# Performance work log

Measured on AMD Instinct MI355X. Metric: run time of the kernel, lower is better.

Reference implementation:

```python
import jax, jax.numpy as jnp
import numpy as np
from jax import lax

WIN = 7
PAD = WIN // 2
K1, K2 = 0.01, 0.03
NP = WIN * WIN
COV_NORM = NP / (NP - 1)  # use_sample_covariance=True


def _dwconv(x, w, channel):
    # depthwise 2D conv, SAME-style explicit padding (torch conv2d padding=pad)
    return lax.conv_general_dilated(
        x, w, window_strides=(1, 1),
        padding=[(PAD, PAD), (PAD, PAD)],
        feature_group_count=channel,
        dimension_numbers=('NCHW', 'OIHW', 'NCHW'))


def setup_inputs() -> dict:
    key = jax.random.key(0)
    k1, k2 = jax.random.split(key)
    B, C, H, W = 64, 1, 384, 384
    gt = jax.random.uniform(k1, (B, C, H, W), dtype=jnp.float32)
    pred = jax.random.uniform(k2, (B, C, H, W), dtype=jnp.float32)
    # uniform (box) window: create_window(7, channel=1, gaussian_weights=False)
    window = jnp.ones((C, 1, WIN, WIN), dtype=jnp.float32) / NP
    return {"gt": gt, "pred": pred, "window": window}


def reference(gt, pred, window):
    channel = gt.shape[1]
    data_range = jnp.max(gt)  # data_range=None default

    ux = _dwconv(gt, window, channel)
    uy = _dwconv(pred, window, channel)
    uxx = _dwconv(gt * gt, window, channel) - ux * ux
    uyy = _dwconv(pred * pred, window, channel) - uy * uy
    uxy = _dwconv(gt * pred, window, channel) - ux * uy

    vx = COV_NORM * uxx
    vy = COV_NORM * uyy
    vxy = COV_NORM * uxy

    C1 = (K1 * data_range) ** 2
    C2 = (K2 * data_range) ** 2

    S = (2.0 * ux * uy + C1) * (2.0 * vxy + C2) / ((ux * ux + uy * uy + C1) * (vx + vy + C2))
    ssim_map = S[:, :, PAD:-PAD, PAD:-PAD]
    return jnp.mean(ssim_map)  # size_average=True, full=False
```

## Files before the change

kernel.cpp:

```cpp
#include <hip/hip_runtime.h>


#define PADW 3
#define BT 256
#define WPB 4
#define BAND 24
#define SROWS (BAND + 6)

constexpr int B_ = 64, H_ = 384, W_ = 384;
constexpr int W2 = W_ / 2;
constexpr int OUTD = W_ - 2 * PADW;
constexpr int NBANDS = 16;
constexpr int NBGRP  = NBANDS / WPB;
constexpr int NTILES = 3;
constexpr int TOTAL_PART = NTILES * NBANDS * B_;
constexpr double NPIX = (double)B_ * OUTD * OUTD;

__device__ __forceinline__ unsigned enc_f(float f) {
    unsigned u = __float_as_uint(f);
    return (u & 0x80000000u) ? ~u : (u | 0x80000000u);
}
__device__ __forceinline__ float dec_f(unsigned e) {
    return __uint_as_float((e & 0x80000000u) ? (e & 0x7fffffffu) : ~e);
}

__device__ __forceinline__ float2 f2add(float2 a, float2 b) { return make_float2(a.x + b.x, a.y + b.y); }
__device__ __forceinline__ float2 f2sub(float2 a, float2 b) { return make_float2(a.x - b.x, a.y - b.y); }

__global__ void __launch_bounds__(256)
max_kernel(const float4* __restrict__ g4, unsigned* ws_max, int n4) {
    int tid = blockIdx.x * blockDim.x + threadIdx.x;
    int stride = gridDim.x * blockDim.x;
    float m = -3.402823466e38f;
    for (int i = tid; i < n4; i += stride) {
        float4 v = g4[i];
        m = fmaxf(m, fmaxf(fmaxf(v.x, v.y), fmaxf(v.z, v.w)));
    }
#pragma unroll
    for (int off = 32; off > 0; off >>= 1)
        m = fmaxf(m, __shfl_down(m, off));
    __shared__ float sm[4];
    if ((threadIdx.x & 63) == 0) sm[threadIdx.x >> 6] = m;
    __syncthreads();
    if (threadIdx.x == 0) {
        float mm = fmaxf(fmaxf(sm[0], sm[1]), fmaxf(sm[2], sm[3]));
        atomicMax(ws_max, enc_f(mm));
    }
}

__device__ __forceinline__ void ssim_nd(float a, float b, float sxx, float syy, float sxy,
                                        float C1q, float C2q, float& num, float& den) {
    const float covn = 49.0f / 48.0f;
    float ab   = a * b;
    float num1 = fmaf(2.0f, ab, C1q);
    float txy  = fmaf(49.0f, sxy, -ab);
    float num2 = fmaf(2.0f * covn, txy, C2q);
    float b2   = b * b;
    float aabb = fmaf(a, a, b2);
    float den1 = aabb + C1q;
    float spq  = sxx + syy;
    float tv   = fmaf(49.0f, spq, -aabb);
    float den2 = fmaf(covn, tv, C2q);
    num = num1 * num2;
    den = den1 * den2;
}

__global__ void __launch_bounds__(BT, 3)
ssim_kernel(const float* __restrict__ gt, const float* __restrict__ pred,
            const unsigned* __restrict__ ws_max, double* __restrict__ ws_part) {
    const int t    = threadIdx.x;
    const int lane = t & 63;
    const int wave = t >> 6;
    const int tile = blockIdx.x;
    const int band = blockIdx.y * WPB + wave;
    const int b    = blockIdx.z;
    const int bid  = (b * NBANDS + band) * NTILES + tile;

    const float dr  = dec_f(*ws_max);
    const float c1  = 0.01f * dr, c2 = 0.03f * dr;
    const float C1q = c1 * c1 * 2401.0f;
    const float C2q = c2 * c2 * 2401.0f;

    const int  row0   = band * BAND;
    const bool active = (lane < 63);

    const int tb = min(tile * 63 + lane, W2 - 4);

    const float2* gp = (const float2*)(gt   + (size_t)b * H_ * W_) + tb;
    const float2* pp = (const float2*)(pred + (size_t)b * H_ * W_) + tb;

    float2 rx[7], ry[7], rxx[7], ryy[7], rxy[7];
#pragma unroll
    for (int j = 0; j < 7; ++j) {
        rx[j] = make_float2(0.f, 0.f); ry[j] = rx[j];
        rxx[j] = rx[j]; ryy[j] = rx[j]; rxy[j] = rx[j];
    }
    float2 vx = make_float2(0.f, 0.f), vy = vx, vxx = vx, vyy = vx, vxy = vx;
    float acc = 0.0f;

    auto dorow = [&](int i, int slot) {
        const int ir = min(row0 + i, H_ - 1);
        const float2* gr = gp + (size_t)ir * W2;
        const float2* pr = pp + (size_t)ir * W2;
        float2 d0 = gr[0], d1 = gr[1], d2 = gr[2], d3 = gr[3];
        float2 e0 = pr[0], e1 = pr[1], e2 = pr[2], e3 = pr[3];

        float hx0 = d0.x + d0.y + d1.x + d1.y + d2.x + d2.y + d3.x;
        float hy0 = e0.x + e0.y + e1.x + e1.y + e2.x + e2.y + e3.x;
        float hxx0 = fmaf(d0.x, d0.x, fmaf(d0.y, d0.y, fmaf(d1.x, d1.x,
                     fmaf(d1.y, d1.y, fmaf(d2.x, d2.x, fmaf(d2.y, d2.y, d3.x * d3.x))))));
        float hyy0 = fmaf(e0.x, e0.x, fmaf(e0.y, e0.y, fmaf(e1.x, e1.x,
                     fmaf(e1.y, e1.y, fmaf(e2.x, e2.x, fmaf(e2.y, e2.y, e3.x * e3.x))))));
        float hxy0 = fmaf(d0.x, e0.x, fmaf(d0.y, e0.y, fmaf(d1.x, e1.x,
                     fmaf(d1.y, e1.y, fmaf(d2.x, e2.x, fmaf(d2.y, e2.y, d3.x * e3.x))))));

        float2 h_x  = make_float2(hx0,  hx0  - d0.x        + d3.y);
        float2 h_y  = make_float2(hy0,  hy0  - e0.x        + e3.y);
        float2 h_xx = make_float2(hxx0, hxx0 - d0.x * d0.x + d3.y * d3.y);
        float2 h_yy = make_float2(hyy0, hyy0 - e0.x * e0.x + e3.y * e3.y);
        float2 h_xy = make_float2(hxy0, hxy0 - d0.x * e0.x + d3.y * e3.y);

        vx  = f2add(vx,  f2sub(h_x,  rx[slot]));  rx[slot]  = h_x;
        vy  = f2add(vy,  f2sub(h_y,  ry[slot]));  ry[slot]  = h_y;
        vxx = f2add(vxx, f2sub(h_xx, rxx[slot])); rxx[slot] = h_xx;
        vyy = f2add(vyy, f2sub(h_yy, ryy[slot])); ryy[slot] = h_yy;
        vxy = f2add(vxy, f2sub(h_xy, rxy[slot])); rxy[slot] = h_xy;

        const int orow = row0 + i - 6;
        if (i >= 6 && active && orow < OUTD) {
            float na, da, nb, db;
            ssim_nd(vx.x, vy.x, vxx.x, vyy.x, vxy.x, C1q, C2q, na, da);
            ssim_nd(vx.y, vy.y, vxx.y, vyy.y, vxy.y, C1q, C2q, nb, db);
            acc += fmaf(na, db, nb * da) / (da * db);
        }
    };

#pragma unroll 1
    for (int g = 0; g < 4; ++g) {
#pragma unroll
        for (int j = 0; j < 7; ++j) dorow(g * 7 + j, j);
    }
    dorow(28, 0);
    dorow(29, 1);

#pragma unroll
    for (int off2 = 32; off2 > 0; off2 >>= 1)
        acc += __shfl_down(acc, off2);
    if (lane == 0) ws_part[bid] = (double)acc;
}

__global__ void __launch_bounds__(256)
final_kernel(const double* __restrict__ ws_part, float* __restrict__ out) {
    const int t = threadIdx.x;
    double s = 0.0;
    for (int i = t; i < TOTAL_PART; i += 256) s += ws_part[i];
#pragma unroll
    for (int off = 32; off > 0; off >>= 1)
        s += __shfl_down(s, off);
    __shared__ double sd[4];
    if ((t & 63) == 0) sd[t >> 6] = s;
    __syncthreads();
    if (t == 0) out[0] = (float)((sd[0] + sd[1] + sd[2] + sd[3]) / NPIX);
}

extern "C" void kernel_launch(void* const* d_in, const int* in_sizes, int n_in,
                              void* d_out, int out_size, void* d_ws, size_t ws_size,
                              hipStream_t stream) {
    const float* gt   = (const float*)d_in[0];
    const float* pred = (const float*)d_in[1];
    float* out = (float*)d_out;

    unsigned* ws_max  = (unsigned*)d_ws;
    double*   ws_part = (double*)((char*)d_ws + 64);


    const int n4 = B_ * H_ * W_ / 4;
    max_kernel<<<1024, 256, 0, stream>>>((const float4*)gt, ws_max, n4);

    dim3 grid(NTILES, NBGRP, B_);
    ssim_kernel<<<grid, BT, 0, stream>>>(gt, pred, ws_max, ws_part);

    final_kernel<<<1, 256, 0, stream>>>(ws_part, out);
}
```

Before: 131.2 us.

## Replace register ring buffer with reloading evicted rows, one wave per block

Removes the 7-slot per-row horizontal-sum ring buffer held in registers. The row leaving the vertical window is now reloaded from memory and its horizontal sums recomputed, which cuts register pressure and should raise occupancy. Blocks become single 64-thread waves, each covering a 14-row band (OUTD/BAND = 27 bands instead of 16), so there are more independent blocks. The cost is about twice the global/L2 loads and double the horizontal-sum arithmetic per row, plus a larger halo fraction from the smaller bands.

Result: slower. 149.6 us (+14.0%).

```diff
diff --git a/kernel.cpp b/kernel.cpp
--- a/kernel.cpp
+++ b/kernel.cpp
@@ -2,16 +2,14 @@
 
 
 #define PADW 3
-#define BT 256
-#define WPB 4
-#define BAND 24
+#define BT 64
+#define BAND 14
 #define SROWS (BAND + 6)
 
 constexpr int B_ = 64, H_ = 384, W_ = 384;
 constexpr int W2 = W_ / 2;
 constexpr int OUTD = W_ - 2 * PADW;
-constexpr int NBANDS = 16;
-constexpr int NBGRP  = NBANDS / WPB;
+constexpr int NBANDS = OUTD / BAND;
 constexpr int NTILES = 3;
 constexpr int TOTAL_PART = NTILES * NBANDS * B_;
 constexpr double NPIX = (double)B_ * OUTD * OUTD;
@@ -65,14 +63,12 @@
     den = den1 * den2;
 }
 
-__global__ void __launch_bounds__(BT, 3)
+__global__ void __launch_bounds__(BT)
 ssim_kernel(const float* __restrict__ gt, const float* __restrict__ pred,
             const unsigned* __restrict__ ws_max, double* __restrict__ ws_part) {
-    const int t    = threadIdx.x;
-    const int lane = t & 63;
-    const int wave = t >> 6;
+    const int lane = threadIdx.x;
     const int tile = blockIdx.x;
-    const int band = blockIdx.y * WPB + wave;
+    const int band = blockIdx.y;
     const int b    = blockIdx.z;
     const int bid  = (b * NBANDS + band) * NTILES + tile;
 
@@ -84,26 +80,23 @@
     const int  row0   = band * BAND;
     const bool active = (lane < 63);
 
-    const int tb = min(tile * 63 + lane, W2 - 4);
+    const int tb  = min(tile * 63 + lane, W2 - 4);
+    const int tb2 = 2 * tb;
 
-    const float2* gp = (const float2*)(gt   + (size_t)b * H_ * W_) + tb;
-    const float2* pp = (const float2*)(pred + (size_t)b * H_ * W_) + tb;
+    const float* gimg = gt   + (size_t)b * H_ * W_;
+    const float* pimg = pred + (size_t)b * H_ * W_;
 
-    float2 rx[7], ry[7], rxx[7], ryy[7], rxy[7];
-#pragma unroll
-    for (int j = 0; j < 7; ++j) {
-        rx[j] = make_float2(0.f, 0.f); ry[j] = rx[j];
-        rxx[j] = rx[j]; ryy[j] = rx[j]; rxy[j] = rx[j];
-    }
     float2 vx = make_float2(0.f, 0.f), vy = vx, vxx = vx, vyy = vx, vxy = vx;
     float acc = 0.0f;
 
-    auto dorow = [&](int i, int slot) {
-        const int ir = min(row0 + i, H_ - 1);
-        const float2* gr = gp + (size_t)ir * W2;
-        const float2* pr = pp + (size_t)ir * W2;
-        float2 d0 = gr[0], d1 = gr[1], d2 = gr[2], d3 = gr[3];
-        float2 e0 = pr[0], e1 = pr[1], e2 = pr[2], e3 = pr[3];
+    auto loadh = [&](int off, float2& Hx, float2& Hy,
+                     float2& Hxx, float2& Hyy, float2& Hxy) {
+        const float* gb = gimg + off + tb2;
+        const float* pb = pimg + off + tb2;
+        float2 d0 = *(const float2*)(gb + 0), d1 = *(const float2*)(gb + 2),
+               d2 = *(const float2*)(gb + 4), d3 = *(const float2*)(gb + 6);
+        float2 e0 = *(const float2*)(pb + 0), e1 = *(const float2*)(pb + 2),
+               e2 = *(const float2*)(pb + 4), e3 = *(const float2*)(pb + 6);
 
         float hx0 = d0.x + d0.y + d1.x + d1.y + d2.x + d2.y + d3.x;
         float hy0 = e0.x + e0.y + e1.x + e1.y + e2.x + e2.y + e3.x;
@@ -114,20 +107,15 @@
         float hxy0 = fmaf(d0.x, e0.x, fmaf(d0.y, e0.y, fmaf(d1.x, e1.x,
                      fmaf(d1.y, e1.y, fmaf(d2.x, e2.x, fmaf(d2.y, e2.y, d3.x * e3.x))))));
 
-        float2 h_x  = make_float2(hx0,  hx0  - d0.x        + d3.y);
-        float2 h_y  = make_float2(hy0,  hy0  - e0.x        + e3.y);
-        float2 h_xx = make_float2(hxx0, hxx0 - d0.x * d0.x + d3.y * d3.y);
-        float2 h_yy = make_float2(hyy0, hyy0 - e0.x * e0.x + e3.y * e3.y);
-        float2 h_xy = make_float2(hxy0, hxy0 - d0.x * e0.x + d3.y * e3.y);
+        Hx  = make_float2(hx0,  hx0  - d0.x        + d3.y);
+        Hy  = make_float2(hy0,  hy0  - e0.x        + e3.y);
+        Hxx = make_float2(hxx0, hxx0 - d0.x * d0.x + d3.y * d3.y);
+        Hyy = make_float2(hyy0, hyy0 - e0.x * e0.x + e3.y * e3.y);
+        Hxy = make_float2(hxy0, hxy0 - d0.x * e0.x + d3.y * e3.y);
+    };
 
-        vx  = f2add(vx,  f2sub(h_x,  rx[slot]));  rx[slot]  = h_x;
-        vy  = f2add(vy,  f2sub(h_y,  ry[slot]));  ry[slot]  = h_y;
-        vxx = f2add(vxx, f2sub(h_xx, rxx[slot])); rxx[slot] = h_xx;
-        vyy = f2add(vyy, f2sub(h_yy, ryy[slot])); ryy[slot] = h_yy;
-        vxy = f2add(vxy, f2sub(h_xy, rxy[slot])); rxy[slot] = h_xy;
-
-        const int orow = row0 + i - 6;
-        if (i >= 6 && active && orow < OUTD) {
+    auto emit = [&]() {
+        if (active) {
             float na, da, nb, db;
             ssim_nd(vx.x, vy.x, vxx.x, vyy.x, vxy.x, C1q, C2q, na, da);
             ssim_nd(vx.y, vy.y, vxx.y, vyy.y, vxy.y, C1q, C2q, nb, db);
@@ -135,13 +123,32 @@
         }
     };
 
+    int co = row0 * W_;
+
+#pragma unroll
+    for (int i = 0; i < 7; ++i) {
+        float2 hx, hy, hxx, hyy, hxy;
+        loadh(co, hx, hy, hxx, hyy, hxy);
+        vx = f2add(vx, hx); vy = f2add(vy, hy); vxx = f2add(vxx, hxx);
+        vyy = f2add(vyy, hyy); vxy = f2add(vxy, hxy);
+        co += W_;
+    }
+    emit();
+
 #pragma unroll 1
-    for (int g = 0; g < 4; ++g) {
-#pragma unroll
-        for (int j = 0; j < 7; ++j) dorow(g * 7 + j, j);
+    for (int i = 7; i < SROWS; ++i) {
+        float2 nx, ny, nxx, nyy, nxy;
+        float2 ex, ey, exx, eyy, exy;
+        loadh(co,            nx, ny, nxx, nyy, nxy);
+        loadh(co - 7 * W_,   ex, ey, exx, eyy, exy);
+        vx  = f2add(vx,  f2sub(nx,  ex));
+        vy  = f2add(vy,  f2sub(ny,  ey));
+        vxx = f2add(vxx, f2sub(nxx, exx));
+        vyy = f2add(vyy, f2sub(nyy, eyy));
+        vxy = f2add(vxy, f2sub(nxy, exy));
+        emit();
+        co += W_;
     }
-    dorow(28, 0);
-    dorow(29, 1);
 
 #pragma unroll
     for (int off2 = 32; off2 > 0; off2 >>= 1)
@@ -177,7 +184,7 @@
     const int n4 = B_ * H_ * W_ / 4;
     max_kernel<<<1024, 256, 0, stream>>>((const float4*)gt, ws_max, n4);
 
-    dim3 grid(NTILES, NBGRP, B_);
+    dim3 grid(NTILES, NBANDS, B_);
     ssim_kernel<<<grid, BT, 0, stream>>>(gt, pred, ws_max, ws_part);
 
     final_kernel<<<1, 256, 0, stream>>>(ws_part, out);
```

## Compute four output columns per thread and recompute evicted rows instead of ring buffer

Applied to the files above, without the earlier changes.

Restructures the SSIM kernel so each thread owns four adjacent output columns across the full image width (128 threads per band, one block per band). The per-column ring buffer of row sums is replaced by recomputing the horizontal sums of the row leaving the vertical window. This cuts register pressure, and the four SSIM terms are merged under a single division. The cost is twice the row loads and horizontal arithmetic per step, plus a different grid shape with fewer, smaller blocks.

Result: slower. 136.9 us (+4.3%).

```diff
diff --git a/kernel.cpp b/kernel.cpp
--- a/kernel.cpp
+++ b/kernel.cpp
@@ -2,18 +2,14 @@
 
 
 #define PADW 3
-#define BT 256
-#define WPB 4
+#define BT 128
 #define BAND 24
 #define SROWS (BAND + 6)
 
 constexpr int B_ = 64, H_ = 384, W_ = 384;
-constexpr int W2 = W_ / 2;
 constexpr int OUTD = W_ - 2 * PADW;
 constexpr int NBANDS = 16;
-constexpr int NBGRP  = NBANDS / WPB;
-constexpr int NTILES = 3;
-constexpr int TOTAL_PART = NTILES * NBANDS * B_;
+constexpr int TOTAL_PART = NBANDS * B_ * 2;
 constexpr double NPIX = (double)B_ * OUTD * OUTD;
 
 __device__ __forceinline__ unsigned enc_f(float f) {
@@ -23,9 +19,6 @@
 __device__ __forceinline__ float dec_f(unsigned e) {
     return __uint_as_float((e & 0x80000000u) ? (e & 0x7fffffffu) : ~e);
 }
-
-__device__ __forceinline__ float2 f2add(float2 a, float2 b) { return make_float2(a.x + b.x, a.y + b.y); }
-__device__ __forceinline__ float2 f2sub(float2 a, float2 b) { return make_float2(a.x - b.x, a.y - b.y); }
 
 __global__ void __launch_bounds__(256)
 max_kernel(const float4* __restrict__ g4, unsigned* ws_max, int n4) {
@@ -65,83 +58,111 @@
     den = den1 * den2;
 }
 
-__global__ void __launch_bounds__(BT, 3)
+__global__ void __launch_bounds__(BT)
 ssim_kernel(const float* __restrict__ gt, const float* __restrict__ pred,
             const unsigned* __restrict__ ws_max, double* __restrict__ ws_part) {
     const int t    = threadIdx.x;
     const int lane = t & 63;
-    const int wave = t >> 6;
-    const int tile = blockIdx.x;
-    const int band = blockIdx.y * WPB + wave;
+    const int wid  = t >> 6;
+    const int band = blockIdx.y;
     const int b    = blockIdx.z;
-    const int bid  = (b * NBANDS + band) * NTILES + tile;
+    const int bid  = (b * NBANDS + band) * 2 + wid;
 
     const float dr  = dec_f(*ws_max);
     const float c1  = 0.01f * dr, c2 = 0.03f * dr;
     const float C1q = c1 * c1 * 2401.0f;
     const float C2q = c2 * c2 * 2401.0f;
 
-    const int  row0   = band * BAND;
-    const bool active = (lane < 63);
-
-    const int tb = min(tile * 63 + lane, W2 - 4);
-
-    const float2* gp = (const float2*)(gt   + (size_t)b * H_ * W_) + tb;
-    const float2* pp = (const float2*)(pred + (size_t)b * H_ * W_) + tb;
-
-    float2 rx[7], ry[7], rxx[7], ryy[7], rxy[7];
-#pragma unroll
-    for (int j = 0; j < 7; ++j) {
-        rx[j] = make_float2(0.f, 0.f); ry[j] = rx[j];
-        rxx[j] = rx[j]; ryy[j] = rx[j]; rxy[j] = rx[j];
-    }
-    float2 vx = make_float2(0.f, 0.f), vy = vx, vxx = vx, vyy = vx, vxy = vx;
+    const int row0 = band * BAND;
+
+    const int oc = min(4 * t, W_ - 10);
+    bool keepc[4];
+#pragma unroll
+    for (int k = 0; k < 4; ++k)
+        keepc[k] = (oc + k >= 4 * t) && (oc + k < OUTD);
+
+    const float* gimg = gt   + (size_t)b * H_ * W_;
+    const float* pimg = pred + (size_t)b * H_ * W_;
+
+    float vx[4], vy[4], vxx[4], vyy[4], vxy[4];
+#pragma unroll
+    for (int k = 0; k < 4; ++k) { vx[k]=0.f; vy[k]=0.f; vxx[k]=0.f; vyy[k]=0.f; vxy[k]=0.f; }
     float acc = 0.0f;
 
-    auto dorow = [&](int i, int slot) {
-        const int ir = min(row0 + i, H_ - 1);
-        const float2* gr = gp + (size_t)ir * W2;
-        const float2* pr = pp + (size_t)ir * W2;
-        float2 d0 = gr[0], d1 = gr[1], d2 = gr[2], d3 = gr[3];
-        float2 e0 = pr[0], e1 = pr[1], e2 = pr[2], e3 = pr[3];
-
-        float hx0 = d0.x + d0.y + d1.x + d1.y + d2.x + d2.y + d3.x;
-        float hy0 = e0.x + e0.y + e1.x + e1.y + e2.x + e2.y + e3.x;
-        float hxx0 = fmaf(d0.x, d0.x, fmaf(d0.y, d0.y, fmaf(d1.x, d1.x,
-                     fmaf(d1.y, d1.y, fmaf(d2.x, d2.x, fmaf(d2.y, d2.y, d3.x * d3.x))))));
-        float hyy0 = fmaf(e0.x, e0.x, fmaf(e0.y, e0.y, fmaf(e1.x, e1.x,
-                     fmaf(e1.y, e1.y, fmaf(e2.x, e2.x, fmaf(e2.y, e2.y, e3.x * e3.x))))));
-        float hxy0 = fmaf(d0.x, e0.x, fmaf(d0.y, e0.y, fmaf(d1.x, e1.x,
-                     fmaf(d1.y, e1.y, fmaf(d2.x, e2.x, fmaf(d2.y, e2.y, d3.x * e3.x))))));
-
-        float2 h_x  = make_float2(hx0,  hx0  - d0.x        + d3.y);
-        float2 h_y  = make_float2(hy0,  hy0  - e0.x        + e3.y);
-        float2 h_xx = make_float2(hxx0, hxx0 - d0.x * d0.x + d3.y * d3.y);
-        float2 h_yy = make_float2(hyy0, hyy0 - e0.x * e0.x + e3.y * e3.y);
-        float2 h_xy = make_float2(hxy0, hxy0 - d0.x * e0.x + d3.y * e3.y);
-
-        vx  = f2add(vx,  f2sub(h_x,  rx[slot]));  rx[slot]  = h_x;
-        vy  = f2add(vy,  f2sub(h_y,  ry[slot]));  ry[slot]  = h_y;
-        vxx = f2add(vxx, f2sub(h_xx, rxx[slot])); rxx[slot] = h_xx;
-        vyy = f2add(vyy, f2sub(h_yy, ryy[slot])); ryy[slot] = h_yy;
-        vxy = f2add(vxy, f2sub(h_xy, rxy[slot])); rxy[slot] = h_xy;
-
-        const int orow = row0 + i - 6;
-        if (i >= 6 && active && orow < OUTD) {
-            float na, da, nb, db;
-            ssim_nd(vx.x, vy.x, vxx.x, vyy.x, vxy.x, C1q, C2q, na, da);
-            ssim_nd(vx.y, vy.y, vxx.y, vyy.y, vxy.y, C1q, C2q, nb, db);
-            acc += fmaf(na, db, nb * da) / (da * db);
+    auto calc = [&](int ir, float hx[4], float hy[4],
+                    float hxx[4], float hyy[4], float hxy[4]) {
+        const float* gp_ = gimg + ir * W_ + oc;
+        const float* pp_ = pimg + ir * W_ + oc;
+        float tp[10], up[10];
+#pragma unroll
+        for (int m = 0; m < 5; ++m) {
+            float2 a  = *(const float2*)(gp_ + 2 * m);
+            float2 b2 = *(const float2*)(pp_ + 2 * m);
+            tp[2*m] = a.x;  tp[2*m+1] = a.y;
+            up[2*m] = b2.x; up[2*m+1] = b2.y;
+        }
+        float sx = tp[0], sy = up[0];
+        float sxx = tp[0]*tp[0], syy = up[0]*up[0], sxy = tp[0]*up[0];
+#pragma unroll
+        for (int m = 1; m < 7; ++m) {
+            sx += tp[m]; sy += up[m];
+            sxx = fmaf(tp[m], tp[m], sxx);
+            syy = fmaf(up[m], up[m], syy);
+            sxy = fmaf(tp[m], up[m], sxy);
+        }
+        hx[0]=sx; hy[0]=sy; hxx[0]=sxx; hyy[0]=syy; hxy[0]=sxy;
+#pragma unroll
+        for (int k = 1; k < 4; ++k) {
+            sx  = sx - tp[k-1] + tp[k+6];
+            sy  = sy - up[k-1] + up[k+6];
+            sxx = fmaf(tp[k+6], tp[k+6], fmaf(-tp[k-1], tp[k-1], sxx));
+            syy = fmaf(up[k+6], up[k+6], fmaf(-up[k-1], up[k-1], syy));
+            sxy = fmaf(tp[k+6], up[k+6], fmaf(-up[k-1], tp[k-1], sxy));
+            hx[k]=sx; hy[k]=sy; hxx[k]=sxx; hyy[k]=syy; hxy[k]=sxy;
         }
     };
 
+    auto emit = [&](int orow) {
+        const bool rowok = orow < OUTD;
+        float n[4], d[4];
+#pragma unroll
+        for (int k = 0; k < 4; ++k) {
+            ssim_nd(vx[k], vy[k], vxx[k], vyy[k], vxy[k], C1q, C2q, n[k], d[k]);
+            n[k] = (rowok && keepc[k]) ? n[k] : 0.0f;
+        }
+        float N01 = fmaf(n[0], d[1], n[1] * d[0]), D01 = d[0] * d[1];
+        float N23 = fmaf(n[2], d[3], n[3] * d[2]), D23 = d[2] * d[3];
+        acc += fmaf(N01, D23, N23 * D01) / (D01 * D23);
+    };
+
+    float hx[4], hy[4], hxx[4], hyy[4], hxy[4];
+    float ex[4], ey[4], exx[4], eyy[4], exy[4];
+
 #pragma unroll 1
-    for (int g = 0; g < 4; ++g) {
-#pragma unroll
-        for (int j = 0; j < 7; ++j) dorow(g * 7 + j, j);
-    }
-    dorow(28, 0);
-    dorow(29, 1);
+    for (int i = 0; i < 7; ++i) {
+        calc(min(row0 + i, H_ - 1), hx, hy, hxx, hyy, hxy);
+#pragma unroll
+        for (int k = 0; k < 4; ++k) {
+            vx[k] += hx[k]; vy[k] += hy[k]; vxx[k] += hxx[k];
+            vyy[k] += hyy[k]; vxy[k] += hxy[k];
+        }
+    }
+    emit(row0);
+
+#pragma unroll 1
+    for (int i = 7; i < SROWS; ++i) {
+        calc(min(row0 + i, H_ - 1),     hx, hy, hxx, hyy, hxy);
+        calc(min(row0 + i - 7, H_ - 1), ex, ey, exx, eyy, exy);
+#pragma unroll
+        for (int k = 0; k < 4; ++k) {
+            vx[k]  += hx[k]  - ex[k];
+            vy[k]  += hy[k]  - ey[k];
+            vxx[k] += hxx[k] - exx[k];
+            vyy[k] += hyy[k] - eyy[k];
+            vxy[k] += hxy[k] - exy[k];
+        }
+        emit(row0 + i - 6);
+    }
 
 #pragma unroll
     for (int off2 = 32; off2 > 0; off2 >>= 1)
@@ -177,7 +198,7 @@
     const int n4 = B_ * H_ * W_ / 4;
     max_kernel<<<1024, 256, 0, stream>>>((const float4*)gt, ws_max, n4);
 
-    dim3 grid(NTILES, NBGRP, B_);
+    dim3 grid(1, NBANDS, B_);
     ssim_kernel<<<grid, BT, 0, stream>>>(gt, pred, ws_max, ws_part);
 
     final_kernel<<<1, 256, 0, stream>>>(ws_part, out);
```
